# Performance work log

Measured on AMD Instinct MI355X. Metric: run time of the kernel, lower is better.

Reference implementation:

```python
import jax, jax.numpy as jnp
import numpy as np

B, L, C_IN = 32, 8192, 64
K, F = 3, 128


def setup_inputs() -> dict:
    key = jax.random.key(0)
    k1, k2 = jax.random.split(key)
    x = jax.random.normal(k1, (B, L, C_IN), dtype=jnp.float32)
    # glorot-ish scale for the conv kernel [k, C_in, F] (TF WIO layout)
    w = jax.random.normal(k2, (K, C_IN, F), dtype=jnp.float32) * (2.0 / (K * C_IN + F)) ** 0.5
    b = jnp.zeros((F,), dtype=jnp.float32)
    return {"x": x, "w": w, "b": b}


def reference(x, w, b):
    # Original: per-position matmul+trace == valid conv1d; then bias + relu.
    # x: [B, L, C_in], w: [K, C_in, F] -> out: [B, L-K+1, F]
    out = jax.lax.conv_general_dilated(
        x, w,
        window_strides=(1,),
        padding="VALID",
        dimension_numbers=("NWC", "WIO", "NWC"),
    )
    return jax.nn.relu(out + b)
```

## Files before the change

### kernel.cpp

```cpp
#include <hip/hip_runtime.h>
#include <hip/hip_bf16.h>

typedef __attribute__((ext_vector_type(8))) short short8;
typedef __attribute__((ext_vector_type(4))) float floatx4;

#define B_SZ   32
#define L_IN   8192
#define C_INCH 64
#define KW     3
#define F_OUT  128
#define L_OUT  (L_IN - KW + 1)
#define KDIM   (KW * C_INCH)

#define TILE_L  64
#define AROWS   (TILE_L + 2)
#define ASTRIDE 72
#define TPB     4
#define NGRID   (B_SZ * (L_IN / TILE_L) / TPB)

__device__ __forceinline__ unsigned pk2(float a, float b) {
    __hip_bfloat162 h = __float22bfloat162_rn(make_float2(a, b));
    unsigned u;
    __builtin_memcpy(&u, &h, 4);
    return u;
}

__global__ __launch_bounds__(256, 3) void conv1d_mfma(const float* __restrict__ x,
                                                      const float* __restrict__ w,
                                                      const float* __restrict__ bias,
                                                      float* __restrict__ out) {
    __shared__ short a_lds[2][AROWS * ASTRIDE];

    const int tid  = threadIdx.x;
    const int lane = tid & 63;
    const int wave = tid >> 6;
    const int q    = lane >> 4;
    const int nl   = lane & 15;

    const int g      = blockIdx.x;
    const int b      = g >> 5;
    const int l_base = (g & 31) * (TPB * TILE_L);

    short8 bfrag[6][2];
#pragma unroll
    for (int n = 0; n < 2; ++n) {
        const int f = (wave * 2 + n) * 16 + nl;
        const float* __restrict__ wf = w + f;
#pragma unroll
        for (int s = 0; s < 6; ++s) {
            float t[8];
#pragma unroll
            for (int j = 0; j < 8; ++j)
                t[j] = wf[(s * 32 + q * 8 + j) * F_OUT];
            union { unsigned u[4]; short8 v; } hb;
            hb.u[0] = pk2(t[0], t[1]);
            hb.u[1] = pk2(t[2], t[3]);
            hb.u[2] = pk2(t[4], t[5]);
            hb.u[3] = pk2(t[6], t[7]);
            bfrag[s][n] = hb.v;
        }
    }

    float bv[2];
#pragma unroll
    for (int n = 0; n < 2; ++n) bv[n] = bias[(wave * 2 + n) * 16 + nl];

    float4 xv0[3], xv1[3];
    {
        const int l0 = l_base;
#pragma unroll
        for (int i = 0; i < 3; ++i) {
            int c = tid + 256 * i;
            if (c < AROWS * 8) {
                int p   = c >> 3;
                int col = (c & 7) * 8;
                int gl  = l0 + p;
                if (gl < L_IN) {
                    const float4* xp =
                        (const float4*)(x + ((size_t)b * L_IN + gl) * C_INCH + col);
                    xv0[i] = xp[0];
                    xv1[i] = xp[1];
                } else {
                    xv0[i] = make_float4(0.f, 0.f, 0.f, 0.f);
                    xv1[i] = xv0[i];
                }
            }
        }
    }

#pragma unroll
    for (int t = 0; t < TPB; ++t) {
        short* buf = a_lds[t & 1];

#pragma unroll
        for (int i = 0; i < 3; ++i) {
            int c = tid + 256 * i;
            if (c < AROWS * 8) {
                int p   = c >> 3;
                int col = (c & 7) * 8;
                union { unsigned u[4]; short8 v; } h;
                h.u[0] = pk2(xv0[i].x, xv0[i].y);
                h.u[1] = pk2(xv0[i].z, xv0[i].w);
                h.u[2] = pk2(xv1[i].x, xv1[i].y);
                h.u[3] = pk2(xv1[i].z, xv1[i].w);
                *(short8*)&buf[p * ASTRIDE + col] = h.v;
            }
        }
        __syncthreads();

        if (t + 1 < TPB) {
            const int l0n = l_base + (t + 1) * TILE_L;
#pragma unroll
            for (int i = 0; i < 3; ++i) {
                int c = tid + 256 * i;
                if (c < AROWS * 8) {
                    int p   = c >> 3;
                    int col = (c & 7) * 8;
                    int gl  = l0n + p;
                    if (gl < L_IN) {
                        const float4* xp =
                            (const float4*)(x + ((size_t)b * L_IN + gl) * C_INCH + col);
                        xv0[i] = xp[0];
                        xv1[i] = xp[1];
                    } else {
                        xv0[i] = make_float4(0.f, 0.f, 0.f, 0.f);
                        xv1[i] = xv0[i];
                    }
                }
            }
        }

        floatx4 acc[4][2];
#pragma unroll
        for (int m = 0; m < 4; ++m)
#pragma unroll
            for (int n = 0; n < 2; ++n) acc[m][n] = (floatx4){0.f, 0.f, 0.f, 0.f};

#pragma unroll
        for (int s = 0; s < 6; ++s) {
#pragma unroll
            for (int m = 0; m < 4; ++m) {
                short8 af = *(const short8*)&buf[(m * 16 + nl + (s >> 1)) * ASTRIDE
                                                 + (s & 1) * 32 + q * 8];
#pragma unroll
                for (int n = 0; n < 2; ++n)
                    acc[m][n] = __builtin_amdgcn_mfma_f32_16x16x32_bf16(
                        af, bfrag[s][n], acc[m][n], 0, 0, 0);
            }
        }

        const int l0 = l_base + t * TILE_L;
#pragma unroll
        for (int n = 0; n < 2; ++n) {
            const int f = (wave * 2 + n) * 16 + nl;
#pragma unroll
            for (int m = 0; m < 4; ++m) {
                const int lb = l0 + m * 16 + q * 4;
#pragma unroll
                for (int r = 0; r < 4; ++r) {
                    int l = lb + r;
                    if (l < L_OUT) {
                        float v = acc[m][n][r] + bv[n];
                        out[((size_t)b * L_OUT + l) * F_OUT + f] = v > 0.f ? v : 0.f;
                    }
                }
            }
        }
    }
}

extern "C" void kernel_launch(void* const* d_in, const int* in_sizes, int n_in,
                              void* d_out, int out_size, void* d_ws, size_t ws_size,
                              hipStream_t stream) {
    const float* x    = (const float*)d_in[0];
    const float* w    = (const float*)d_in[1];
    const float* bias = (const float*)d_in[2];
    float* out        = (float*)d_out;
    (void)d_ws; (void)ws_size;

    conv1d_mfma<<<dim3(NGRID), 256, 0, stream>>>(x, w, bias, out);
}
```

Measured before the change: 213.1 us.

## Prepack weights in a prep kernel, one tile per block, swap MFMA operands for vector stores

Adds a small prep kernel that converts the weights to bf16 MFMA fragments once in the workspace, so each block loads them with coalesced vector loads instead of strided fp32 gathers. Each block now handles one 64-row tile instead of four, which drops the double-buffered prefetch loop and allows 4 blocks per CU. The MFMA operands are swapped so each lane holds 4 consecutive output channels, which turns the scalar epilogue stores into float4 stores and the bias load into a float4 load. In exchange the kernel issues an extra launch and loses the overlap between loading the next tile and computing the current one.

```diff
diff --git a/kernel.cpp b/kernel.cpp
--- a/kernel.cpp
+++ b/kernel.cpp
@@ -15,8 +15,9 @@
 #define TILE_L  64
 #define AROWS   (TILE_L + 2)
 #define ASTRIDE 72
-#define TPB     4
-#define NGRID   (B_SZ * (L_IN / TILE_L) / TPB)
+#define NGRID   (B_SZ * (L_IN / TILE_L))
+
+#define WTAB_ELEMS (8 * 6 * 64)
 
 __device__ __forceinline__ unsigned pk2(float a, float b) {
     __hip_bfloat162 h = __float22bfloat162_rn(make_float2(a, b));
@@ -25,11 +26,33 @@
     return u;
 }
 
-__global__ __launch_bounds__(256, 3) void conv1d_mfma(const float* __restrict__ x,
+__global__ __launch_bounds__(256) void w_prep(const float* __restrict__ w,
+                                              short8* __restrict__ wtab) {
+    int id = blockIdx.x * 256 + threadIdx.x;
+    if (id >= WTAB_ELEMS) return;
+    int lane = id & 63;
+    int s    = (id >> 6) % 6;
+    int nt   = id / 384;
+    int nl = lane & 15, q = lane >> 4;
+    const float* __restrict__ wf = w + nt * 16 + nl;
+    float t[8];
+#pragma unroll
+    for (int j = 0; j < 8; ++j) t[j] = wf[(s * 32 + q * 8 + j) * F_OUT];
+    union { unsigned u[4]; short8 v; } hb;
+    hb.u[0] = pk2(t[0], t[1]);
+    hb.u[1] = pk2(t[2], t[3]);
+    hb.u[2] = pk2(t[4], t[5]);
+    hb.u[3] = pk2(t[6], t[7]);
+    wtab[id] = hb.v;
+}
+
+template <bool PREP>
+__global__ __launch_bounds__(256, 4) void conv1d_mfma(const float* __restrict__ x,
                                                       const float* __restrict__ w,
                                                       const float* __restrict__ bias,
-                                                      float* __restrict__ out) {
-    __shared__ short a_lds[2][AROWS * ASTRIDE];
+                                                      float* __restrict__ out,
+                                                      const short8* __restrict__ wtab) {
+    __shared__ short a_lds[AROWS * ASTRIDE];
 
     const int tid  = threadIdx.x;
     const int lane = tid & 63;
@@ -37,133 +60,106 @@
     const int q    = lane >> 4;
     const int nl   = lane & 15;
 
-    const int g      = blockIdx.x;
-    const int b      = g >> 5;
-    const int l_base = (g & 31) * (TPB * TILE_L);
+    const int g  = blockIdx.x;
+    const int b  = g >> 7;
+    const int l0 = (g & 127) * TILE_L;
 
     short8 bfrag[6][2];
+    if (PREP) {
 #pragma unroll
-    for (int n = 0; n < 2; ++n) {
-        const int f = (wave * 2 + n) * 16 + nl;
-        const float* __restrict__ wf = w + f;
+        for (int n = 0; n < 2; ++n)
 #pragma unroll
-        for (int s = 0; s < 6; ++s) {
-            float t[8];
+            for (int s = 0; s < 6; ++s)
+                bfrag[s][n] = wtab[(((wave * 2 + n) * 6 + s) << 6) + lane];
+    } else {
 #pragma unroll
-            for (int j = 0; j < 8; ++j)
-                t[j] = wf[(s * 32 + q * 8 + j) * F_OUT];
-            union { unsigned u[4]; short8 v; } hb;
-            hb.u[0] = pk2(t[0], t[1]);
-            hb.u[1] = pk2(t[2], t[3]);
-            hb.u[2] = pk2(t[4], t[5]);
-            hb.u[3] = pk2(t[6], t[7]);
-            bfrag[s][n] = hb.v;
-        }
-    }
-
-    float bv[2];
+        for (int n = 0; n < 2; ++n) {
+            const int f = (wave * 2 + n) * 16 + nl;
+            const float* __restrict__ wf = w + f;
 #pragma unroll
-    for (int n = 0; n < 2; ++n) bv[n] = bias[(wave * 2 + n) * 16 + nl];
-
-    float4 xv0[3], xv1[3];
-    {
-        const int l0 = l_base;
+            for (int s = 0; s < 6; ++s) {
+                float t[8];
 #pragma unroll
-        for (int i = 0; i < 3; ++i) {
-            int c = tid + 256 * i;
-            if (c < AROWS * 8) {
-                int p   = c >> 3;
-                int col = (c & 7) * 8;
-                int gl  = l0 + p;
-                if (gl < L_IN) {
-                    const float4* xp =
-                        (const float4*)(x + ((size_t)b * L_IN + gl) * C_INCH + col);
-                    xv0[i] = xp[0];
-                    xv1[i] = xp[1];
-                } else {
-                    xv0[i] = make_float4(0.f, 0.f, 0.f, 0.f);
-                    xv1[i] = xv0[i];
-                }
+                for (int j = 0; j < 8; ++j)
+                    t[j] = wf[(s * 32 + q * 8 + j) * F_OUT];
+                union { unsigned u[4]; short8 v; } hb;
+                hb.u[0] = pk2(t[0], t[1]);
+                hb.u[1] = pk2(t[2], t[3]);
+                hb.u[2] = pk2(t[4], t[5]);
+                hb.u[3] = pk2(t[6], t[7]);
+                bfrag[s][n] = hb.v;
             }
         }
     }
 
+    float4 bv[2];
 #pragma unroll
-    for (int t = 0; t < TPB; ++t) {
-        short* buf = a_lds[t & 1];
+    for (int n = 0; n < 2; ++n)
+        bv[n] = *(const float4*)(bias + (wave * 2 + n) * 16 + q * 4);
 
 #pragma unroll
-        for (int i = 0; i < 3; ++i) {
-            int c = tid + 256 * i;
-            if (c < AROWS * 8) {
-                int p   = c >> 3;
-                int col = (c & 7) * 8;
-                union { unsigned u[4]; short8 v; } h;
-                h.u[0] = pk2(xv0[i].x, xv0[i].y);
-                h.u[1] = pk2(xv0[i].z, xv0[i].w);
-                h.u[2] = pk2(xv1[i].x, xv1[i].y);
-                h.u[3] = pk2(xv1[i].z, xv1[i].w);
-                *(short8*)&buf[p * ASTRIDE + col] = h.v;
+    for (int i = 0; i < 3; ++i) {
+        int c = tid + 256 * i;
+        if (c < AROWS * 8) {
+            int p   = c >> 3;
+            int col = (c & 7) * 8;
+            int gl  = l0 + p;
+            float4 v0, v1;
+            if (gl < L_IN) {
+                const float4* xp =
+                    (const float4*)(x + ((size_t)b * L_IN + gl) * C_INCH + col);
+                v0 = xp[0];
+                v1 = xp[1];
+            } else {
+                v0 = make_float4(0.f, 0.f, 0.f, 0.f);
+                v1 = v0;
             }
+            union { unsigned u[4]; short8 v; } h;
+            h.u[0] = pk2(v0.x, v0.y);
+            h.u[1] = pk2(v0.z, v0.w);
+            h.u[2] = pk2(v1.x, v1.y);
+            h.u[3] = pk2(v1.z, v1.w);
+            *(short8*)&a_lds[p * ASTRIDE + col] = h.v;
         }
-        __syncthreads();
+    }
+    __syncthreads();
 
-        if (t + 1 < TPB) {
-            const int l0n = l_base + (t + 1) * TILE_L;
+    floatx4 acc[4][2];
 #pragma unroll
-            for (int i = 0; i < 3; ++i) {
-                int c = tid + 256 * i;
-                if (c < AROWS * 8) {
-                    int p   = c >> 3;
-                    int col = (c & 7) * 8;
-                    int gl  = l0n + p;
-                    if (gl < L_IN) {
-                        const float4* xp =
-                            (const float4*)(x + ((size_t)b * L_IN + gl) * C_INCH + col);
-                        xv0[i] = xp[0];
-                        xv1[i] = xp[1];
-                    } else {
-                        xv0[i] = make_float4(0.f, 0.f, 0.f, 0.f);
-                        xv1[i] = xv0[i];
-                    }
-                }
-            }
-        }
-
-        floatx4 acc[4][2];
+    for (int m = 0; m < 4; ++m)
 #pragma unroll
-        for (int m = 0; m < 4; ++m)
-#pragma unroll
-            for (int n = 0; n < 2; ++n) acc[m][n] = (floatx4){0.f, 0.f, 0.f, 0.f};
+        for (int n = 0; n < 2; ++n) acc[m][n] = (floatx4){0.f, 0.f, 0.f, 0.f};
 
 #pragma unroll
-        for (int s = 0; s < 6; ++s) {
+    for (int s = 0; s < 6; ++s) {
 #pragma unroll
-            for (int m = 0; m < 4; ++m) {
-                short8 af = *(const short8*)&buf[(m * 16 + nl + (s >> 1)) * ASTRIDE
-                                                 + (s & 1) * 32 + q * 8];
+        for (int m = 0; m < 4; ++m) {
+            short8 af = *(const short8*)&a_lds[(m * 16 + nl + (s >> 1)) * ASTRIDE
+                                               + (s & 1) * 32 + q * 8];
 #pragma unroll
-                for (int n = 0; n < 2; ++n)
-                    acc[m][n] = __builtin_amdgcn_mfma_f32_16x16x32_bf16(
-                        af, bfrag[s][n], acc[m][n], 0, 0, 0);
-            }
+            for (int n = 0; n < 2; ++n)
+                acc[m][n] = __builtin_amdgcn_mfma_f32_16x16x32_bf16(
+                    bfrag[s][n], af, acc[m][n], 0, 0, 0);
         }
+    }
 
-        const int l0 = l_base + t * TILE_L;
 #pragma unroll
-        for (int n = 0; n < 2; ++n) {
-            const int f = (wave * 2 + n) * 16 + nl;
+    for (int n = 0; n < 2; ++n) {
+        const int fb = (wave * 2 + n) * 16 + q * 4;
 #pragma unroll
-            for (int m = 0; m < 4; ++m) {
-                const int lb = l0 + m * 16 + q * 4;
-#pragma unroll
-                for (int r = 0; r < 4; ++r) {
-                    int l = lb + r;
-                    if (l < L_OUT) {
-                        float v = acc[m][n][r] + bv[n];
-                        out[((size_t)b * L_OUT + l) * F_OUT + f] = v > 0.f ? v : 0.f;
-                    }
-                }
+        for (int m = 0; m < 4; ++m) {
+            const int l = l0 + m * 16 + nl;
+            if (l < L_OUT) {
+                float4 v;
+                v.x = acc[m][n][0] + bv[n].x;
+                v.y = acc[m][n][1] + bv[n].y;
+                v.z = acc[m][n][2] + bv[n].z;
+                v.w = acc[m][n][3] + bv[n].w;
+                v.x = v.x > 0.f ? v.x : 0.f;
+                v.y = v.y > 0.f ? v.y : 0.f;
+                v.z = v.z > 0.f ? v.z : 0.f;
+                v.w = v.w > 0.f ? v.w : 0.f;
+                *(float4*)(out + ((size_t)b * L_OUT + l) * F_OUT + fb) = v;
             }
         }
     }
@@ -176,7 +172,12 @@
     const float* w    = (const float*)d_in[1];
     const float* bias = (const float*)d_in[2];
     float* out        = (float*)d_out;
-    (void)d_ws; (void)ws_size;
 
-    conv1d_mfma<<<dim3(NGRID), 256, 0, stream>>>(x, w, bias, out);
+    if (d_ws != nullptr && ws_size >= (size_t)WTAB_ELEMS * sizeof(short8)) {
+        short8* wtab = (short8*)d_ws;
+        w_prep<<<dim3((WTAB_ELEMS + 255) / 256), 256, 0, stream>>>(w, wtab);
+        conv1d_mfma<true><<<dim3(NGRID), 256, 0, stream>>>(x, w, bias, out, wtab);
+    } else {
+        conv1d_mfma<false><<<dim3(NGRID), 256, 0, stream>>>(x, w, bias, out, nullptr);
+    }
 }
```

After: 191.7 us. -10.0%, faster.

## Precompute bf16 weight fragments, swap MFMA operands for vector stores, halve tiles per block

Applied to the files above, without the earlier changes.

Adds a small prep kernel that converts the weights into bf16 MFMA fragments in workspace, so each block loads ready fragments instead of doing strided gathers and conversions. The MFMA operands are swapped so each lane holds four consecutive output channels, which allows 16-byte nontemporal output stores with a vectorized bias load. TPB drops from 4 to 2, doubling the grid, and launch bounds target 4 blocks per CU. The cost is an extra kernel launch plus less amortization of the weight load per block.

```diff
diff --git a/kernel.cpp b/kernel.cpp
--- a/kernel.cpp
+++ b/kernel.cpp
@@ -15,8 +15,10 @@
 #define TILE_L  64
 #define AROWS   (TILE_L + 2)
 #define ASTRIDE 72
-#define TPB     4
+#define TPB     2
 #define NGRID   (B_SZ * (L_IN / TILE_L) / TPB)
+
+#define WTAB_ELEMS (8 * 6 * 64)
 
 __device__ __forceinline__ unsigned pk2(float a, float b) {
     __hip_bfloat162 h = __float22bfloat162_rn(make_float2(a, b));
@@ -25,10 +27,32 @@
     return u;
 }
 
-__global__ __launch_bounds__(256, 3) void conv1d_mfma(const float* __restrict__ x,
+__global__ __launch_bounds__(256) void w_prep(const float* __restrict__ w,
+                                              short8* __restrict__ wtab) {
+    int id = blockIdx.x * 256 + threadIdx.x;
+    if (id >= WTAB_ELEMS) return;
+    int lane = id & 63;
+    int s    = (id >> 6) % 6;
+    int nt   = id / 384;
+    int nl = lane & 15, q = lane >> 4;
+    const float* __restrict__ wf = w + nt * 16 + nl;
+    float t[8];
+#pragma unroll
+    for (int j = 0; j < 8; ++j) t[j] = wf[(s * 32 + q * 8 + j) * F_OUT];
+    union { unsigned u[4]; short8 v; } hb;
+    hb.u[0] = pk2(t[0], t[1]);
+    hb.u[1] = pk2(t[2], t[3]);
+    hb.u[2] = pk2(t[4], t[5]);
+    hb.u[3] = pk2(t[6], t[7]);
+    wtab[id] = hb.v;
+}
+
+template <bool PREP>
+__global__ __launch_bounds__(256, 4) void conv1d_mfma(const float* __restrict__ x,
                                                       const float* __restrict__ w,
                                                       const float* __restrict__ bias,
-                                                      float* __restrict__ out) {
+                                                      float* __restrict__ out,
+                                                      const short8* __restrict__ wtab) {
     __shared__ short a_lds[2][AROWS * ASTRIDE];
 
     const int tid  = threadIdx.x;
@@ -38,32 +62,41 @@
     const int nl   = lane & 15;
 
     const int g      = blockIdx.x;
-    const int b      = g >> 5;
-    const int l_base = (g & 31) * (TPB * TILE_L);
+    const int b      = g >> 6;
+    const int l_base = (g & 63) * (TPB * TILE_L);
 
     short8 bfrag[6][2];
-#pragma unroll
-    for (int n = 0; n < 2; ++n) {
-        const int f = (wave * 2 + n) * 16 + nl;
-        const float* __restrict__ wf = w + f;
-#pragma unroll
-        for (int s = 0; s < 6; ++s) {
-            float t[8];
-#pragma unroll
-            for (int j = 0; j < 8; ++j)
-                t[j] = wf[(s * 32 + q * 8 + j) * F_OUT];
-            union { unsigned u[4]; short8 v; } hb;
-            hb.u[0] = pk2(t[0], t[1]);
-            hb.u[1] = pk2(t[2], t[3]);
-            hb.u[2] = pk2(t[4], t[5]);
-            hb.u[3] = pk2(t[6], t[7]);
-            bfrag[s][n] = hb.v;
-        }
-    }
-
-    float bv[2];
-#pragma unroll
-    for (int n = 0; n < 2; ++n) bv[n] = bias[(wave * 2 + n) * 16 + nl];
+    if (PREP) {
+#pragma unroll
+        for (int n = 0; n < 2; ++n)
+#pragma unroll
+            for (int s = 0; s < 6; ++s)
+                bfrag[s][n] = wtab[(((wave * 2 + n) * 6 + s) << 6) + lane];
+    } else {
+#pragma unroll
+        for (int n = 0; n < 2; ++n) {
+            const int f = (wave * 2 + n) * 16 + nl;
+            const float* __restrict__ wf = w + f;
+#pragma unroll
+            for (int s = 0; s < 6; ++s) {
+                float t[8];
+#pragma unroll
+                for (int j = 0; j < 8; ++j)
+                    t[j] = wf[(s * 32 + q * 8 + j) * F_OUT];
+                union { unsigned u[4]; short8 v; } hb;
+                hb.u[0] = pk2(t[0], t[1]);
+                hb.u[1] = pk2(t[2], t[3]);
+                hb.u[2] = pk2(t[4], t[5]);
+                hb.u[3] = pk2(t[6], t[7]);
+                bfrag[s][n] = hb.v;
+            }
+        }
+    }
+
+    float4 bv[2];
+#pragma unroll
+    for (int n = 0; n < 2; ++n)
+        bv[n] = *(const float4*)(bias + (wave * 2 + n) * 16 + q * 4);
 
     float4 xv0[3], xv1[3];
     {
@@ -145,24 +178,29 @@
 #pragma unroll
                 for (int n = 0; n < 2; ++n)
                     acc[m][n] = __builtin_amdgcn_mfma_f32_16x16x32_bf16(
-                        af, bfrag[s][n], acc[m][n], 0, 0, 0);
+                        bfrag[s][n], af, acc[m][n], 0, 0, 0);
             }
         }
 
         const int l0 = l_base + t * TILE_L;
 #pragma unroll
         for (int n = 0; n < 2; ++n) {
-            const int f = (wave * 2 + n) * 16 + nl;
+            const int fb = (wave * 2 + n) * 16 + q * 4;
 #pragma unroll
             for (int m = 0; m < 4; ++m) {
-                const int lb = l0 + m * 16 + q * 4;
-#pragma unroll
-                for (int r = 0; r < 4; ++r) {
-                    int l = lb + r;
-                    if (l < L_OUT) {
-                        float v = acc[m][n][r] + bv[n];
-                        out[((size_t)b * L_OUT + l) * F_OUT + f] = v > 0.f ? v : 0.f;
-                    }
+                const int l = l0 + m * 16 + nl;
+                if (l < L_OUT) {
+                    floatx4 v;
+                    v[0] = acc[m][n][0] + bv[n].x;
+                    v[1] = acc[m][n][1] + bv[n].y;
+                    v[2] = acc[m][n][2] + bv[n].z;
+                    v[3] = acc[m][n][3] + bv[n].w;
+                    v[0] = v[0] > 0.f ? v[0] : 0.f;
+                    v[1] = v[1] > 0.f ? v[1] : 0.f;
+                    v[2] = v[2] > 0.f ? v[2] : 0.f;
+                    v[3] = v[3] > 0.f ? v[3] : 0.f;
+                    __builtin_nontemporal_store(
+                        v, (floatx4*)(out + ((size_t)b * L_OUT + l) * F_OUT + fb));
                 }
             }
         }
@@ -176,7 +214,12 @@
     const float* w    = (const float*)d_in[1];
     const float* bias = (const float*)d_in[2];
     float* out        = (float*)d_out;
-    (void)d_ws; (void)ws_size;
-
-    conv1d_mfma<<<dim3(NGRID), 256, 0, stream>>>(x, w, bias, out);
-}
+
+    if (d_ws != nullptr && ws_size >= (size_t)WTAB_ELEMS * sizeof(short8)) {
+        short8* wtab = (short8*)d_ws;
+        w_prep<<<dim3((WTAB_ELEMS + 255) / 256), 256, 0, stream>>>(w, wtab);
+        conv1d_mfma<true><<<dim3(NGRID), 256, 0, stream>>>(x, w, bias, out, wtab);
+    } else {
+        conv1d_mfma<false><<<dim3(NGRID), 256, 0, stream>>>(x, w, bias, out, nullptr);
+    }
+}
```

After: 211.6 us. No clear change (-0.7%).
